# Kernel tuning notes

Hardware: AMD Instinct MI355X
Metric: run time of the kernel (lower is better)

## Reference

```python
import jax, jax.numpy as jnp
import numpy as np

TOPK, ALPHA, BETA, EPS = 13, 1.0, 6.0, 1e-9


def setup_inputs() -> dict:
    key = jax.random.key(0)
    k0, k1, k2, k3, k4, k5 = jax.random.split(key, 6)
    bs, C, A = 64, 80, 8400
    pd_scores = jax.random.uniform(k0, (bs, C, A), dtype=jnp.float32)
    # predicted boxes in x1y1x2y2 (normalized coords), guaranteed x2>x1, y2>y1
    xy1 = jax.random.uniform(k1, (bs, 2, A), dtype=jnp.float32) * 0.6
    wh = jax.random.uniform(k2, (bs, 2, A), dtype=jnp.float32) * 0.4 + 0.01
    pd_bboxes = jnp.concatenate([xy1, xy1 + wh], axis=1)  # (bs,4,A)
    gxy1 = jax.random.uniform(k3, (bs, 2), dtype=jnp.float32) * 0.6
    gwh = jax.random.uniform(k4, (bs, 2), dtype=jnp.float32) * 0.4 + 0.01
    gt_bboxes = jnp.concatenate([gxy1, gxy1 + gwh], axis=1)  # (bs,4)
    gt_labels = jax.random.randint(k5, (64,), 0, C)
    return {"pd_scores": pd_scores, "pd_bboxes": pd_bboxes,
            "gt_labels": gt_labels, "gt_bboxes": gt_bboxes}


def reference(pd_scores, pd_bboxes, gt_labels, gt_bboxes):
    bs, _, num_anchors = pd_scores.shape
    # ---- IoU: gt (bs,4,1) vs pred (bs,4,A) -> (bs,A)
    b1 = gt_bboxes[:, :, None]                       # (bs,4,1)
    px1y1, px2y2 = b1[:, 0:2], b1[:, 2:4]            # (bs,2,1)
    gx1y1, gx2y2 = pd_bboxes[:, 0:2], pd_bboxes[:, 2:4]  # (bs,2,A)
    overlap = jnp.clip(jnp.minimum(px2y2, gx2y2) - jnp.maximum(px1y1, gx1y1), 0).prod(axis=-2)  # (bs,A)
    area1 = jnp.clip(px2y2 - px1y1, 0).prod(axis=-2)  # (bs,1)
    area2 = jnp.clip(gx2y2 - gx1y1, 0).prod(axis=-2)  # (bs,A)
    overlaps = overlap / (area1 + area2 - overlap + EPS)  # (bs,A)
    # ---- alignment metric
    bbox_scores = pd_scores[jnp.arange(bs), gt_labels]  # (bs,A) gather per-image class row
    align_metric = (bbox_scores ** ALPHA) * (overlaps ** BETA)
    # ---- top-k candidate mask (scatter instead of one_hot+sum)
    topk_metrics, topk_idxs = jax.lax.top_k(align_metric, TOPK)   # (bs,TOPK)
    topk_mask = topk_metrics.max(axis=-1, keepdims=True) > EPS    # (bs,1)
    topk_idxs = jnp.where(topk_mask, topk_idxs, 0)
    cnt = jnp.zeros((bs, num_anchors), jnp.int32).at[
        jnp.arange(bs)[:, None], topk_idxs].add(1)
    mask_pos = jnp.where(cnt > 1, 0, cnt).astype(align_metric.dtype)  # (bs,A)
    # ---- normalized target scores (faithful to original reduction axes)
    am = align_metric * mask_pos
    pos_align_metrics = am.max(axis=-1, keepdims=True)            # (bs,1)
    pos_overlaps = (overlaps * mask_pos).max(axis=-1, keepdims=True)  # (bs,1)
    norm_align_metric = (am * pos_overlaps / (pos_align_metrics + EPS)).max(axis=-2)[:, None]  # (A,1)
    target_scores = gt_labels.astype(norm_align_metric.dtype) * norm_align_metric  # (A,bs)
    return target_scores, mask_pos
```

## Files before the change

kernel.cpp:

```cpp
#include <hip/hip_runtime.h>
#include <hip/hip_bf16.h>

#define NA 8400
#define BS 64
#define NC 80
#define TOPK 13
#define EPSF 1e-9f
#define SEG 2100
#define KMAX 33

__global__ __launch_bounds__(256) void assign_kernel(
    const float* __restrict__ pd_scores,
    const float* __restrict__ pd_bboxes,
    const int*   __restrict__ gt_labels,
    const float* __restrict__ gt_bboxes,
    float*       __restrict__ out_mask,
    float*       __restrict__ norm)
{
    __shared__ float s_cv[4 * TOPK];
    __shared__ int   s_ci[4 * TOPK];
    __shared__ float s_cov[4 * TOPK];
    __shared__ int   s_win[TOPK];
    __shared__ float s_mask;

    const int b = blockIdx.x;
    const int t = threadIdx.x;
    const int wave = t >> 6, lane = t & 63;
    const int seg_lo = wave * SEG;
    const int seg_hi = seg_lo + SEG;

    const float p1x = gt_bboxes[b * 4 + 0];
    const float p1y = gt_bboxes[b * 4 + 1];
    const float p2x = gt_bboxes[b * 4 + 2];
    const float p2y = gt_bboxes[b * 4 + 3];
    const float area1 = fmaxf(p2x - p1x, 0.f) * fmaxf(p2y - p1y, 0.f);
    const int lbl = gt_labels[b];
    const float* sc = pd_scores + (size_t)b * NC * NA + (size_t)lbl * NA;
    const float* bb = pd_bboxes + (size_t)b * 4 * NA;

    float lv[KMAX], lov[KMAX];
    #pragma unroll
    for (int k = 0; k < KMAX; ++k) {
        int a = seg_lo + lane + (k << 6);
        bool ok = a < seg_hi;
        int aa = ok ? a : seg_lo;
        float g1x = bb[0 * NA + aa];
        float g1y = bb[1 * NA + aa];
        float g2x = bb[2 * NA + aa];
        float g2y = bb[3 * NA + aa];
        float wx = fmaxf(fminf(p2x, g2x) - fmaxf(p1x, g1x), 0.f);
        float wy = fmaxf(fminf(p2y, g2y) - fmaxf(p1y, g1y), 0.f);
        float ovl = wx * wy;
        float area2 = fmaxf(g2x - g1x, 0.f) * fmaxf(g2y - g1y, 0.f);
        float o = ovl / (area1 + area2 - ovl + EPSF);
        float o2 = o * o;
        float score = sc[aa];
        lv[k]  = ok ? score * (o2 * o2 * o2) : -1.0f;
        lov[k] = o;
    }

    unsigned long long selmask = 0ULL;
    float cand_v = -2.f; int cand_i = 0x7fffffff; float cand_ov = 0.f;
    for (int j = 0; j < TOPK; ++j) {
        float mv = -2.f; int mk = 0; float mov = 0.f;
        #pragma unroll
        for (int k = 0; k < KMAX; ++k) {
            bool excl = (selmask >> k) & 1ULL;
            float v = excl ? -2.f : lv[k];
            if (v > mv) { mv = v; mk = k; mov = lov[k]; }
        }
        int mi = seg_lo + lane + (mk << 6);
        float bv = mv; int bi = mi; float bov = mov;
        #pragma unroll
        for (int off = 1; off < 64; off <<= 1) {
            float ov_ = __shfl_xor(bv, off);
            int   oi_ = __shfl_xor(bi, off);
            float oo_ = __shfl_xor(bov, off);
            if (ov_ > bv || (ov_ == bv && oi_ < bi)) { bv = ov_; bi = oi_; bov = oo_; }
        }
        if (mi == bi) selmask |= 1ULL << mk;
        if (lane == j) { cand_v = bv; cand_i = bi; cand_ov = bov; }
    }
    if (lane < TOPK) {
        s_cv [wave * TOPK + lane] = cand_v;
        s_ci [wave * TOPK + lane] = cand_i;
        s_cov[wave * TOPK + lane] = cand_ov;
    }
    __syncthreads();

    if (wave == 0) {
        const int NC4 = 4 * TOPK;
        float v  = lane < NC4 ? s_cv[lane]  : -2.f;
        int   ci = lane < NC4 ? s_ci[lane]  : 0x7fffffff;
        float ov = lane < NC4 ? s_cov[lane] : 0.f;
        float pos_align = 0.f, pos_ov = 0.f;
        float wv_sel = 0.f; int wi_sel = 0;
        for (int j = 0; j < TOPK; ++j) {
            float bv = v; int bi = ci; float bov = ov;
            #pragma unroll
            for (int off = 1; off < 64; off <<= 1) {
                float ov_ = __shfl_xor(bv, off);
                int   oi_ = __shfl_xor(bi, off);
                float oo_ = __shfl_xor(bov, off);
                if (ov_ > bv || (ov_ == bv && oi_ < bi)) { bv = ov_; bi = oi_; bov = oo_; }
            }
            if (j == 0) pos_align = bv;
            pos_ov = fmaxf(pos_ov, bov);
            if (lane == j) { wv_sel = bv; wi_sel = bi; }
            if (ci == bi) v = -2.f;
        }
        float mask = pos_align > EPSF ? 1.f : 0.f;
        if (lane == 0) s_mask = mask;
        if (lane < TOPK) {
            s_win[lane] = wi_sel;
            if (mask != 0.f) {
                float vv = (wv_sel * pos_ov) / (pos_align + EPSF);
                atomicMax((int*)&norm[wi_sel], __float_as_int(vv));
            }
        }
    }
    __syncthreads();

    const float maskf = s_mask;
    int w0  = s_win[0],  w1  = s_win[1],  w2  = s_win[2],  w3 = s_win[3];
    int w4  = s_win[4],  w5  = s_win[5],  w6  = s_win[6],  w7 = s_win[7];
    int w8  = s_win[8],  w9  = s_win[9],  w10 = s_win[10], w11 = s_win[11];
    int w12 = s_win[12];
    float* om = out_mask + (size_t)b * NA;
    #pragma unroll
    for (int k = 0; k < KMAX; ++k) {
        int a = seg_lo + lane + (k << 6);
        if (a < seg_hi) {
            bool sel = (a == w0) | (a == w1) | (a == w2) | (a == w3) |
                       (a == w4) | (a == w5) | (a == w6) | (a == w7) |
                       (a == w8) | (a == w9) | (a == w10) | (a == w11) |
                       (a == w12);
            om[a] = (sel && maskf > 0.5f) ? 1.0f : 0.0f;
        }
    }
}

__global__ __launch_bounds__(256) void scores_kernel(
    const float* __restrict__ norm,
    const int*   __restrict__ gt_labels,
    float*       __restrict__ out0)
{
    int idx = blockIdx.x * 256 + threadIdx.x;
    if (idx >= NA * BS) return;
    int b = idx & (BS - 1);
    int a = idx >> 6;
    out0[idx] = (float)gt_labels[b] * norm[a];
}

extern "C" void kernel_launch(void* const* d_in, const int* in_sizes, int n_in,
                              void* d_out, int out_size, void* d_ws, size_t ws_size,
                              hipStream_t stream) {
    const float* pd_scores = (const float*)d_in[0];
    const float* pd_bboxes = (const float*)d_in[1];
    const int*   gt_labels = (const int*)d_in[2];
    const float* gt_bboxes = (const float*)d_in[3];

    float* out0     = (float*)d_out;
    float* out_mask = out0 + (size_t)NA * BS;
    float* norm     = (float*)d_ws;

    hipMemsetAsync(norm, 0, NA * sizeof(float), stream);
    assign_kernel<<<BS, 256, 0, stream>>>(pd_scores, pd_bboxes, gt_labels,
                                          gt_bboxes, out_mask, norm);
    scores_kernel<<<(NA * BS + 255) / 256, 256, 0, stream>>>(norm, gt_labels, out0);
}
```

Baseline: 265.5 us.

## Tree-reduce per-thread argmax and replace global atomics with per-block winner scatter

The per-lane top-k argmax over 33 register values changes from a serial scan into a pairwise tree reduction, which shortens the dependency chain in each of the 13 selection rounds. The global memset plus atomicMax on the norm array is removed. Each image now writes its 13 winners and values to workspace, and every scores block rebuilds its 80-anchor slice of norm with shared-memory atomics before writing its outputs. This drops one launch and the global atomics, but each scores block now scans all 832 winner entries.

```diff
diff --git a/kernel.cpp b/kernel.cpp
--- a/kernel.cpp
+++ b/kernel.cpp
@@ -15,7 +15,8 @@
     const int*   __restrict__ gt_labels,
     const float* __restrict__ gt_bboxes,
     float*       __restrict__ out_mask,
-    float*       __restrict__ norm)
+    float*       __restrict__ ws_v,
+    int*         __restrict__ ws_i)
 {
     __shared__ float s_cv[4 * TOPK];
     __shared__ int   s_ci[4 * TOPK];
@@ -62,15 +63,36 @@
     unsigned long long selmask = 0ULL;
     float cand_v = -2.f; int cand_i = 0x7fffffff; float cand_ov = 0.f;
     for (int j = 0; j < TOPK; ++j) {
-        float mv = -2.f; int mk = 0; float mov = 0.f;
+        float tv[17]; int tk[17]; float tvo[17];
         #pragma unroll
-        for (int k = 0; k < KMAX; ++k) {
-            bool excl = (selmask >> k) & 1ULL;
-            float v = excl ? -2.f : lv[k];
-            if (v > mv) { mv = v; mk = k; mov = lov[k]; }
-        }
-        int mi = seg_lo + lane + (mk << 6);
-        float bv = mv; int bi = mi; float bov = mov;
+        for (int i = 0; i < 16; ++i) {
+            int k0 = 2 * i, k1 = 2 * i + 1;
+            float v0 = ((selmask >> k0) & 1ULL) ? -2.f : lv[k0];
+            float v1 = ((selmask >> k1) & 1ULL) ? -2.f : lv[k1];
+            bool take0 = v0 >= v1;
+            tv[i]  = take0 ? v0 : v1;
+            tk[i]  = take0 ? k0 : k1;
+            tvo[i] = take0 ? lov[k0] : lov[k1];
+        }
+        tv[16]  = ((selmask >> 32) & 1ULL) ? -2.f : lv[32];
+        tk[16]  = 32;
+        tvo[16] = lov[32];
+        #pragma unroll
+        for (int n = 17; n > 1; n = (n + 1) / 2) {
+            #pragma unroll
+            for (int i = 0; i < n / 2; ++i) {
+                int i0 = 2 * i, i1 = 2 * i + 1;
+                bool take0 = (tv[i0] > tv[i1]) ||
+                             (tv[i0] == tv[i1] && tk[i0] < tk[i1]);
+                tv[i]  = take0 ? tv[i0]  : tv[i1];
+                tk[i]  = take0 ? tk[i0]  : tk[i1];
+                tvo[i] = take0 ? tvo[i0] : tvo[i1];
+            }
+            if (n & 1) { tv[n / 2] = tv[n - 1]; tk[n / 2] = tk[n - 1]; tvo[n / 2] = tvo[n - 1]; }
+        }
+        int   mk = tk[0];
+        int   mi = seg_lo + lane + (mk << 6);
+        float bv = tv[0]; int bi = mi; float bov = tvo[0];
         #pragma unroll
         for (int off = 1; off < 64; off <<= 1) {
             float ov_ = __shfl_xor(bv, off);
@@ -113,10 +135,9 @@
         if (lane == 0) s_mask = mask;
         if (lane < TOPK) {
             s_win[lane] = wi_sel;
-            if (mask != 0.f) {
-                float vv = (wv_sel * pos_ov) / (pos_align + EPSF);
-                atomicMax((int*)&norm[wi_sel], __float_as_int(vv));
-            }
+            float vv = (mask != 0.f) ? (wv_sel * pos_ov) / (pos_align + EPSF) : 0.f;
+            ws_v[b * TOPK + lane] = vv;
+            ws_i[b * TOPK + lane] = wi_sel;
         }
     }
     __syncthreads();
@@ -140,16 +161,36 @@
     }
 }
 
+#define ABLK 80
 __global__ __launch_bounds__(256) void scores_kernel(
-    const float* __restrict__ norm,
+    const float* __restrict__ ws_v,
+    const int*   __restrict__ ws_i,
     const int*   __restrict__ gt_labels,
     float*       __restrict__ out0)
 {
-    int idx = blockIdx.x * 256 + threadIdx.x;
-    if (idx >= NA * BS) return;
-    int b = idx & (BS - 1);
-    int a = idx >> 6;
-    out0[idx] = (float)gt_labels[b] * norm[a];
+    __shared__ int   s_norm[ABLK];
+    __shared__ float s_lbl[BS];
+
+    const int t  = threadIdx.x;
+    const int a0 = blockIdx.x * ABLK;
+
+    if (t < ABLK) s_norm[t] = 0;
+    if (t < BS)   s_lbl[t]  = (float)gt_labels[t];
+    __syncthreads();
+
+    #pragma unroll
+    for (int e = t; e < BS * TOPK; e += 256) {
+        int idx = ws_i[e];
+        unsigned r = (unsigned)(idx - a0);
+        if (r < ABLK) atomicMax(&s_norm[r], __float_as_int(ws_v[e]));
+    }
+    __syncthreads();
+
+    float* o = out0 + (size_t)a0 * BS;
+    #pragma unroll
+    for (int i = t; i < ABLK * BS; i += 256) {
+        o[i] = s_lbl[i & (BS - 1)] * __int_as_float(s_norm[i >> 6]);
+    }
 }
 
 extern "C" void kernel_launch(void* const* d_in, const int* in_sizes, int n_in,
@@ -162,10 +203,10 @@
 
     float* out0     = (float*)d_out;
     float* out_mask = out0 + (size_t)NA * BS;
-    float* norm     = (float*)d_ws;
-
-    hipMemsetAsync(norm, 0, NA * sizeof(float), stream);
+    float* ws_v     = (float*)d_ws;
+    int*   ws_i     = (int*)((char*)d_ws + BS * TOPK * sizeof(float));
+
     assign_kernel<<<BS, 256, 0, stream>>>(pd_scores, pd_bboxes, gt_labels,
-                                          gt_bboxes, out_mask, norm);
-    scores_kernel<<<(NA * BS + 255) / 256, 256, 0, stream>>>(norm, gt_labels, out0);
+                                          gt_bboxes, out_mask, ws_v, ws_i);
+    scores_kernel<<<NA / ABLK, 256, 0, stream>>>(ws_v, ws_i, gt_labels, out0);
 }
```

Result: slower. 308.3 us (+16.2%).
